# Performance work log

Measured on AMD Instinct MI355X. Metric: run time of the kernel, lower is better.

## Reference

```python
import jax, jax.numpy as jnp
import numpy as np

J = 3
J_H = 5
C_IN = 128
C_OUT = 128
N0, N1, N2 = 1024, 3072, 2048
DENSITY = 0.01
W_SCALE = 0.02  # keeps P^(2^(J_h-1)) @ x @ W magnitudes reasonable in fp32


def _sym_sparse(key, n, density):
    kv, km = jax.random.split(key)
    mask = jax.random.uniform(km, (n, n)) < density
    a = jnp.where(mask, jax.random.normal(kv, (n, n)), 0.0)
    return jnp.triu(a) + jnp.triu(a, 1).T  # symmetric sparse 'Laplacian'


def _sparse(kv, km, shape, density):
    mask = jax.random.uniform(km, shape) < density
    return jnp.where(mask, jax.random.normal(kv, shape), 0.0)


def setup_inputs() -> dict:
    key = jax.random.key(0)
    ks = jax.random.split(key, 24)
    z0 = jax.random.normal(ks[0], (N0, C_IN), jnp.float32)
    z1 = jax.random.normal(ks[1], (N1, C_IN), jnp.float32)
    z2 = jax.random.normal(ks[2], (N2, C_IN), jnp.float32)
    L0 = _sym_sparse(ks[3], N0, 0.02)
    L1_d = _sym_sparse(ks[4], N1, DENSITY)
    L1_u = _sym_sparse(ks[5], N1, DENSITY)
    L2 = _sym_sparse(ks[6], N2, DENSITY)
    B1 = _sparse(ks[7], ks[8], (N0, N1), DENSITY)
    B2 = _sparse(ks[9], ks[10], (N1, N2), DENSITY)
    W_d = jax.random.normal(ks[11], (J, C_IN, C_OUT)) * W_SCALE
    W_u = jax.random.normal(ks[12], (J, C_IN, C_OUT)) * W_SCALE
    W_h = jax.random.normal(ks[13], (C_IN, C_OUT)) * W_SCALE
    W_b1 = jax.random.normal(ks[14], (J, C_IN, C_OUT)) * W_SCALE
    W_b2 = jax.random.normal(ks[15], (J, C_IN, C_OUT)) * W_SCALE
    attn_d_w = jax.random.normal(ks[16], (1, 2 * C_IN)) * W_SCALE
    attn_d_b = jax.random.normal(ks[17], (1,)) * W_SCALE
    attn_u_w = jax.random.normal(ks[18], (1, 2 * C_IN)) * W_SCALE
    attn_u_b = jax.random.normal(ks[19], (1,)) * W_SCALE
    return dict(z0=z0, z1=z1, z2=z2, L0=L0, L1_d=L1_d, L1_u=L1_u, L2=L2,
                B1=B1, B2=B2, W_d=W_d, W_u=W_u, W_h=W_h, W_b1=W_b1, W_b2=W_b2,
                attn_d_w=attn_d_w, attn_d_b=attn_d_b,
                attn_u_w=attn_u_w, attn_u_b=attn_u_b)


def _attention(x, n, w, b, src, dst):
    # gather edge endpoints -> tiny MLP -> sigmoid -> symmetric scatter
    a = jnp.concatenate([x[src], x[dst]], axis=-1)      # [E, 2C]
    s = jax.nn.sigmoid(a @ w.T + b)[:, 0]               # [E]
    return jnp.zeros((n, n), x.dtype).at[src, dst].set(s).at[dst, src].set(s)


def _harmonic(L, x, W_h):
    lmax = jnp.linalg.eigvalsh(L)[-1]
    # torch does lambda_max.item() -> constant w.r.t. grads
    eps = jax.lax.stop_gradient(jnp.where(lmax > 0, 1.0 / lmax, 0.1))
    P = jnp.eye(L.shape[0], dtype=x.dtype) - eps * L
    for _ in range(J_H - 1):
        P = P @ P                                        # P^(2^(J_h-1))
    return P @ x @ W_h


def reference(z0, z1, z2, L0, L1_d, L1_u, L2, B1, B2,
              W_d, W_u, W_h, W_b1, W_b2,
              attn_d_w, attn_d_b, attn_u_w, attn_u_b):
    # nonzero patterns of the Laplacians (constants, computed on host)
    src_d, dst_d = np.nonzero(np.asarray(jax.device_get(L1_d)))
    src_u, dst_u = np.nonzero(np.asarray(jax.device_get(L1_u)))
    L1d_attn = _attention(z1, N1, attn_d_w, attn_d_b,
                          jnp.asarray(src_d), jnp.asarray(dst_d))
    L1u_attn = _attention(z1, N1, attn_u_w, attn_u_b,
                          jnp.asarray(src_u), jnp.asarray(dst_u))
    # sum_j (A @ z) @ W[j] == (A @ z) @ W.sum(0)
    Wd_s, Wu_s = W_d.sum(0), W_u.sum(0)
    Wb1_s, Wb2_s = W_b1.sum(0), W_b2.sum(0)

    z0_out = (L0 @ z0) @ Wd_s + (B1 @ z1) @ Wb1_s + _harmonic(L0, z0, W_h)
    z0_out = jax.nn.relu(z0_out)

    z1_out = ((L1d_attn @ z1) @ Wd_s + (L1u_attn @ z1) @ Wu_s
              + (B1.T @ z0) @ Wb1_s + (B2 @ z2) @ Wb2_s
              + _harmonic(L1_d + L1_u, z1, W_h))
    z1_out = jax.nn.relu(z1_out)

    z2_out = (L2 @ z2) @ Wu_s + (B2.T @ z1) @ Wb2_s + _harmonic(L2, z2, W_h)
    z2_out = jax.nn.relu(z2_out)
    return (z0_out, z1_out, z2_out)
```

## Files before the change

kernel.cpp:

```cpp
#include <hip/hip_runtime.h>
#include <string.h>

constexpr int M_LZ = 48;

constexpr int CAP_L0 = 26240, CAP_L1 = 118016, CAP_L2 = 52480, CAP_B1 = 39360, CAP_B2 = 78720;
constexpr int CB_L0 = 0;
constexpr int CB_L1D = CB_L0 + CAP_L0;
constexpr int CB_L1U = CB_L1D + CAP_L1;
constexpr int CB_L2  = CB_L1U + CAP_L1;
constexpr int CB_B1  = CB_L2 + CAP_L2;
constexpr int CB_B2  = CB_B1 + CAP_B1;
constexpr int CAP_TOT= CB_B2 + CAP_B2;
constexpr int CB_B1T = CAP_TOT;
constexpr int CB_B2T = CB_B1T + CAP_B1;
constexpr int CAP_TOT2 = CB_B2T + CAP_B2;

constexpr int P_L0=0, P_L1D=1025, P_L1U=4098, P_L2=7171, P_B1=9220, P_B2=10245;
constexpr int P_B1T=13320, P_B2T=16393;
constexpr int C_L0=0, C_L1D=1024, C_L1U=4096, C_L2=7168, C_B1=9216, C_B2=10240;
constexpr int C_B1T=13312, C_B2T=16384;

constexpr size_t HBUF  = (size_t)6144*128;

constexpr size_t W_CNT = 0;
constexpr size_t W_PTR = 18432;
constexpr size_t W_CUR = W_PTR + 18444;
constexpr size_t W_CIDX= W_CUR + 5120;
constexpr size_t W_VAL = W_CIDX + CAP_TOT2;
constexpr size_t W_V0  = W_VAL + CAP_TOT2;
constexpr size_t W_PK  = W_V0 + 6144;
constexpr size_t W_TT  = W_PK + (size_t)64*6144*4;
constexpr size_t W_EPS = W_TT + 6144;
constexpr size_t W_UV  = W_EPS + 128;
constexpr size_t W_H   = W_UV + 4*3072;
constexpr size_t W_SCAT= W_H + 15*HBUF;
constexpr size_t S0_OFF= 0;
constexpr size_t S1_OFF= (size_t)1024*384;
constexpr size_t S2_OFF= S1_OFF + (size_t)3072*640;
constexpr size_t SCAT_TOT = S2_OFF + (size_t)2048*384;
constexpr size_t W_WCAT= W_SCAT + SCAT_TOT;
constexpr size_t WC0=0, WC1=(size_t)384*128, WC2=WC1+(size_t)640*128;
constexpr size_t W_SLOT= W_WCAT + (size_t)1408*128;
constexpr size_t W_FLG = W_SLOT + 1048576;
constexpr size_t W_REL = W_FLG + 65536;

__device__ __forceinline__ float wredf(float v){
  #pragma unroll
  for(int o=32;o;o>>=1) v += __shfl_xor(v,o,64);
  return v;
}
__device__ __forceinline__ int wredi(int v){
  #pragma unroll
  for(int o=32;o;o>>=1) v += __shfl_xor(v,o,64);
  return v;
}

__device__ __forceinline__ float ldc(const float* p){
  return __hip_atomic_load(p, __ATOMIC_RELAXED, __HIP_MEMORY_SCOPE_AGENT);
}
__device__ __forceinline__ float2 ldc2(const float* p){
  unsigned long long u = __hip_atomic_load((const unsigned long long*)p,
                          __ATOMIC_RELAXED, __HIP_MEMORY_SCOPE_AGENT);
  float2 r; memcpy(&r,&u,8); return r;
}
__device__ __forceinline__ void stc(float* p, float v){
  __hip_atomic_store(p, v, __ATOMIC_RELAXED, __HIP_MEMORY_SCOPE_AGENT);
}
__device__ __forceinline__ void stc2(float* p, float2 v){
  unsigned long long u; memcpy(&u,&v,8);
  __hip_atomic_store((unsigned long long*)p, u, __ATOMIC_RELAXED, __HIP_MEMORY_SCOPE_AGENT);
}
__device__ __forceinline__ int ldci(const int* p){
  return __hip_atomic_load(p, __ATOMIC_RELAXED, __HIP_MEMORY_SCOPE_AGENT);
}
__device__ __forceinline__ void stci(int* p, int v){
  __hip_atomic_store(p, v, __ATOMIC_RELAXED, __HIP_MEMORY_SCOPE_AGENT);
}

__device__ __forceinline__ void barg(float* ws, int* leafs, int b, int lbase, int Ng,
                                     bool chk, int lidx, int ph){
  const int t = threadIdx.x;
  int* flg = (int*)ws + W_FLG;
  __builtin_amdgcn_s_waitcnt(0);
  __syncthreads();
  if (t==0) stci(flg + (size_t)b*32, ph+1);
  if (chk){
    for (int s=t; s<Ng; s+=256){
      const int* f = flg + (size_t)(lbase+s)*32;
      while (ldci(f) < ph+1) __builtin_amdgcn_s_sleep(1);
    }
    __syncthreads();
    if (t==0){
      #pragma unroll
      for (int i=0;i<16;i++) stci(leafs + (size_t)i*32, ph+1);
    }
    __syncthreads();
  } else {
    if (t==0){
      const int* rl = leafs + (size_t)(lidx&15)*32;
      while (ldci(rl) < ph+1) __builtin_amdgcn_s_sleep(1);
    }
    __syncthreads();
  }
}

__device__ __forceinline__ void bar_lz(float* ws, int b, int grp, int lbase, int Lg,
                                       bool chk, int lb, int ph, int j,
                                       float* shr, float* redm,
                                       float& a_o, float& g_o, float& ib_o){
  const int t = threadIdx.x, lane = t&63, wvv = t>>6;
  __builtin_amdgcn_s_waitcnt(0);
  __syncthreads();
  if (t==0){
    float A0=redm[0]+redm[1]+redm[2]+redm[3];
    float G0=redm[4]+redm[5]+redm[6]+redm[7];
    float N0=redm[8]+redm[9]+redm[10]+redm[11];
    float* sl = ws + W_SLOT + ((size_t)j*2048 + b)*8;
    stc2(sl+2, make_float2(A0,G0)); stc(sl+4, N0);
    __builtin_amdgcn_s_waitcnt(0);
    stci((int*)sl, ph+1);
  }
  if (chk){
    float pa=0.f, pg=0.f, pn=0.f;
    for (int s=t; s<Lg; s+=256){
      const float* sl = ws + W_SLOT + ((size_t)j*2048 + lbase+s)*8;
      while (ldci((const int*)sl) < ph+1) __builtin_amdgcn_s_sleep(1);
      float2 ag = ldc2(sl+2); float nn = ldc(sl+4);
      pa+=ag.x; pg+=ag.y; pn+=nn;
    }
    pa=wredf(pa); pg=wredf(pg); pn=wredf(pn);
    if (lane==0){ shr[0*4+wvv]=pa; shr[1*4+wvv]=pg; shr[2*4+wvv]=pn; }
    __syncthreads();
    if (t==0){
      float a=shr[0]+shr[1]+shr[2]+shr[3];
      float g=shr[4]+shr[5]+shr[6]+shr[7];
      float n=shr[8]+shr[9]+shr[10]+shr[11];
      float ib = 1.f/sqrtf(fmaxf(n - a*a - g*g, 1e-20f));
      float* TT = ws + W_TT + (size_t)(grp*64 + j)*32;
      stc2(TT, make_float2(a,g)); stc(TT+2, n);
      #pragma unroll
      for (int i=0;i<16;i++){
        float* lf = ws + W_REL + (size_t)(grp*16+i)*32;
        stc2(lf+2, make_float2(a,g)); stc(lf+4, ib);
      }
      __builtin_amdgcn_s_waitcnt(0);
      #pragma unroll
      for (int i=0;i<16;i++)
        stci((int*)(ws + W_REL) + (size_t)(grp*16+i)*32, ph+1);
      shr[0]=a; shr[1]=g; shr[2]=ib;
    }
    __syncthreads();
  } else {
    if (t==0){
      const float* lf = ws + W_REL + (size_t)(grp*16 + (lb&15))*32;
      while (ldci((const int*)lf) < ph+1) __builtin_amdgcn_s_sleep(1);
      float2 ag = ldc2(lf+2); float ib = ldc(lf+4);
      shr[0]=ag.x; shr[1]=ag.y; shr[2]=ib;
    }
    __syncthreads();
  }
  a_o = shr[0]; g_o = shr[1]; ib_o = shr[2];
}

__global__ void k_wprep(const float* Wd,const float* Wu,const float* Wh,
                        const float* Wb1,const float* Wb2, float* ws){
  int t = blockIdx.x*256 + threadIdx.x;
  if (t >= 16384) return;
  int* wsi = (int*)ws;
  if (t < 5120) wsi[W_CNT + 13312 + t] = 0;
  if (t < 5120) wsi[W_CUR + t] = 0;
  for (int i=t; i<65536+2048; i+=16384) wsi[W_FLG+i] = 0;
  for (int i=t; i<131072; i+=16384) wsi[W_SLOT + (size_t)i*8] = 0;
  float sd = Wd[t]  + Wd[16384+t]  + Wd[32768+t];
  float su = Wu[t]  + Wu[16384+t]  + Wu[32768+t];
  float s1 = Wb1[t] + Wb1[16384+t] + Wb1[32768+t];
  float s2 = Wb2[t] + Wb2[16384+t] + Wb2[32768+t];
  float wh = Wh[t];
  float* W0 = ws + W_WCAT + WC0;
  float* W1 = ws + W_WCAT + WC1;
  float* W2 = ws + W_WCAT + WC2;
  W0[t]=sd; W0[16384+t]=s1; W0[32768+t]=wh;
  W1[t]=sd; W1[16384+t]=su; W1[32768+t]=s1; W1[49152+t]=s2; W1[65536+t]=wh;
  W2[t]=su; W2[16384+t]=s2; W2[32768+t]=wh;
}

__device__ __forceinline__ void mat_meta(int wid, const float* L0,const float* L1d,const float* L1u,
    const float* L2,const float* B1,const float* B2,
    const float*& M,int& ncol,int& lrow,int& co,int& po,int& cb,int& cap,int& tco){
  if (wid < 1024){ M=L0;  ncol=1024; lrow=wid;        co=C_L0;  po=P_L0;  cb=CB_L0;  cap=CAP_L0; tco=-1; }
  else if (wid < 4096){ M=L1d; ncol=3072; lrow=wid-1024;  co=C_L1D; po=P_L1D; cb=CB_L1D; cap=CAP_L1; tco=-1; }
  else if (wid < 7168){ M=L1u; ncol=3072; lrow=wid-4096;  co=C_L1U; po=P_L1U; cb=CB_L1U; cap=CAP_L1; tco=-1; }
  else if (wid < 9216){ M=L2;  ncol=2048; lrow=wid-7168;  co=C_L2;  po=P_L2;  cb=CB_L2;  cap=CAP_L2; tco=-1; }
  else if (wid < 10240){ M=B1; ncol=3072; lrow=wid-9216;  co=C_B1;  po=P_B1;  cb=CB_B1;  cap=CAP_B1; tco=C_B1T; }
  else { M=B2; ncol=2048; lrow=wid-10240; co=C_B2;  po=P_B2;  cb=CB_B2;  cap=CAP_B2; tco=C_B2T; }
}

__global__ void k_count(const float* L0,const float* L1d,const float* L1u,const float* L2,
                        const float* B1,const float* B2,int* cnt){
  int wid = blockIdx.x*4 + (threadIdx.x>>6);
  int lane = threadIdx.x & 63;
  if (wid >= 13312) return;
  const float* M; int ncol,lrow,co,po,cb,cap,tco;
  mat_meta(wid,L0,L1d,L1u,L2,B1,B2,M,ncol,lrow,co,po,cb,cap,tco);
  const float4* row4 = (const float4*)(M + (size_t)lrow*ncol);
  int c = 0;
  for (int j0=0; j0<ncol; j0+=256){
    float4 v = row4[(j0>>2)+lane];
    int n0=v.x!=0.f, n1=v.y!=0.f, n2=v.z!=0.f, n3=v.w!=0.f;
    c += n0+n1+n2+n3;
    if (tco>=0){
      int jb = j0 + lane*4;
      if (n0) atomicAdd(cnt+tco+jb,   1);
      if (n1) atomicAdd(cnt+tco+jb+1, 1);
      if (n2) atomicAdd(cnt+tco+jb+2, 1);
      if (n3) atomicAdd(cnt+tco+jb+3, 1);
    }
  }
  c = wredi(c);
  if (lane==0) cnt[co+lrow] = c;
}

__global__ void k_prefix(const int* cnt, int* ptr, int* cur){
  __shared__ int lds[257];
  const int rows[8]={1024,3072,3072,2048,1024,3072,3072,2048};
  const int cofs[8]={C_L0,C_L1D,C_L1U,C_L2,C_B1,C_B2,C_B1T,C_B2T};
  const int pofs[8]={P_L0,P_L1D,P_L1U,P_L2,P_B1,P_B2,P_B1T,P_B2T};
  int b=blockIdx.x, t=threadIdx.x;
  int R=rows[b]; const int* c=cnt+cofs[b]; int* p=ptr+pofs[b];
  int* cc = (b==6)? cur : (b==7)? cur+3072 : nullptr;
  int chunk=(R+255)/256;
  int lo=t*chunk, hi=min(R,lo+chunk);
  int s=0;
  for(int i=lo;i<hi;i++) s+=c[i];
  lds[t]=s; __syncthreads();
  if(t==0){ int run=0; for(int i=0;i<256;i++){int x=lds[i];lds[i]=run;run+=x;} lds[256]=run; }
  __syncthreads();
  int run=lds[t];
  for(int i=lo;i<hi;i++){ p[i]=run; if(cc) cc[i]=run; run+=c[i]; }
  if(t==0) p[R]=lds[256];
}

__global__ void k_fill(const float* L0,const float* L1d,const float* L1u,const float* L2,
                       const float* B1,const float* B2,const int* ptr,int* cidx,float* val){
  int wid = blockIdx.x*4 + (threadIdx.x>>6);
  int lane = threadIdx.x & 63;
  if (wid >= 13312) return;
  const float* M; int ncol,lrow,co,po,cb,cap,tco;
  mat_meta(wid,L0,L1d,L1u,L2,B1,B2,M,ncol,lrow,co,po,cb,cap,tco);
  const float4* row4 = (const float4*)(M + (size_t)lrow*ncol);
  int base = ptr[po+lrow];
  int run = 0;
  for (int j0=0; j0<ncol; j0+=256){
    float4 v = row4[(j0>>2)+lane];
    int n0=v.x!=0.f, n1=v.y!=0.f, n2=v.z!=0.f, n3=v.w!=0.f;
    int local = n0+n1+n2+n3;
    int incl = local;
    #pragma unroll
    for (int o=1;o<64;o<<=1){
      int tmp = __shfl_up(incl,o,64);
      if (lane>=o) incl += tmp;
    }
    int tot = __shfl(incl,63,64);
    int pos = base + run + incl - local;
    int jb = j0 + lane*4;
    if (n0){ if(pos<cap){cidx[cb+pos]=jb;   val[cb+pos]=v.x;} pos++; }
    if (n1){ if(pos<cap){cidx[cb+pos]=jb+1; val[cb+pos]=v.y;} pos++; }
    if (n2){ if(pos<cap){cidx[cb+pos]=jb+2; val[cb+pos]=v.z;} pos++; }
    if (n3){ if(pos<cap){cidx[cb+pos]=jb+3; val[cb+pos]=v.w;} pos++; }
    run += tot;
  }
}

__global__ void k_fillT(float* ws){
  int wid = blockIdx.x*4 + (threadIdx.x>>6);
  int lane = threadIdx.x & 63;
  if (wid >= 4096) return;
  int* wsi=(int*)ws;
  const int* ptr=wsi+W_PTR; int* cidx=wsi+W_CIDX; float* val=ws+W_VAL;
  int* cur=wsi+W_CUR;
  if (wid < 1024){
    int r=wid;
    int e=ptr[P_B1+r+1];
    for(int k=ptr[P_B1+r]+lane;k<e;k+=64){
      int c=cidx[CB_B1+k]; float v=val[CB_B1+k];
      int pos=atomicAdd(cur+c,1);
      cidx[CB_B1T+pos]=r; val[CB_B1T+pos]=v;
    }
  } else {
    int r=wid-1024;
    int e=ptr[P_B2+r+1];
    for(int k=ptr[P_B2+r]+lane;k<e;k+=64){
      int c=cidx[CB_B2+k]; float v=val[CB_B2+k];
      int pos=atomicAdd(cur+3072+c,1);
      cidx[CB_B2T+pos]=r; val[CB_B2T+pos]=v;
    }
  }
}

__global__ __launch_bounds__(256,8) void k_solve(float* ws,
    const float* z0,const float* z1,const float* z2,
    const float* adw,const float* adb,const float* auw,const float* aub,
    float* out){
  const int b = blockIdx.x, t = threadIdx.x;
  const int wv = t>>6, lane = t&63;
  const int sg = lane>>4, chn = lane&15;
  const int* wsi=(const int*)ws;
  const int* ptr=wsi+W_PTR; const int* cidx=wsi+W_CIDX; const float* val=ws+W_VAL;

  __shared__ float smem[2616];
  float* Sl  = smem;
  float* Wl  = smem + 544;
  float* TTa = smem;
  float* TTb = smem + 64;
  float* redm= smem + 2592;
  float* shr = smem + 2604;

  int* grel = (int*)ws + W_REL + 48*32;

  { int i = b*256+t;
    if (i < 6144){
      float invs = (i<1024)?0.03125f:(i<4096)?0.0180421959f:0.0220970869f;
      unsigned uu=(unsigned)i*2654435761u; uu^=uu>>16; uu*=2246822519u; uu^=uu>>13;
      stc(ws+W_V0+i, (uu&1)?invs:-invs);
    }
  }
  { int gw = b*4+wv;
    if (gw < 3072){
      float2 x  = ((const float2*)(z1+(size_t)gw*128))[lane];
      float2 a0 = ((const float2*)adw)[lane];
      float2 a1 = ((const float2*)adw)[64+lane];
      float2 b0 = ((const float2*)auw)[lane];
      float2 b1 = ((const float2*)auw)[64+lane];
      float ud=x.x*a0.x+x.y*a0.y, vd=x.x*a1.x+x.y*a1.y;
      float uu=x.x*b0.x+x.y*b0.y, vu=x.x*b1.x+x.y*b1.y;
      ud=wredf(ud); vd=wredf(vd); uu=wredf(uu); vu=wredf(vu);
      if(lane==0){ stc(ws+W_UV+gw,ud); stc(ws+W_UV+3072+gw,vd);
                   stc(ws+W_UV+6144+gw,uu); stc(ws+W_UV+9216+gw,vu); }
    }
  }
  if (b==0 && t<16) stci((int*)ws + W_CNT + (size_t)t*32, 0);
  barg(ws, grel, b, 0, 2048, b==0, b, 0);

  if (b < 768){
    int g, gbase, nb;
    if (b<128){ g=0; gbase=0;   nb=0;    }
    else if (b<512){ g=1; gbase=128; nb=1024; }
    else { g=2; gbase=512; nb=4096; }
    const int lb = b - gbase;
    const int Lg = (g==0)?128:(g==1)?384:256;
    const bool chk = (lb==0);
    const int hw = lane>>5, hl = lane&31;
    const int p  = lb*8 + wv*2 + hw;
    const int gp = nb + p;
    float a=0.f, gmm=0.f, ib=1.f;
    float vp_m1=0.f, vp_m2=0.f, wp_m1=0.f;
    for (int j=0;j<M_LZ;j++){
      float wp=0.f;
      if (j==0){
        const float* v0 = ws + W_V0;
        #define GZ(PP,CBB) { const int* rp=ptr+PP; int e=rp[p+1]; \
          for (int k=rp[p]+hl;k<e;k+=32){ wp += val[CBB+k]*v0[nb+cidx[CBB+k]]; } }
        if (g==0){ GZ(P_L0,CB_L0) }
        else if (g==1){ GZ(P_L1D,CB_L1D) GZ(P_L1U,CB_L1U) }
        else { GZ(P_L2,CB_L2) }
        #undef GZ
      } else {
        const float4* pk = (const float4*)(ws + W_PK) + (size_t)(j-1)*6144 + nb;
        #define GP(PP,CBB) { const int* rp=ptr+PP; int e=rp[p+1]; \
          for (int k=rp[p]+hl;k<e;k+=32){ float v=val[CBB+k]; float4 pq=pk[cidx[CBB+k]]; \
            wp += v*((pq.x - a*pq.y - gmm*pq.z)*ib); } }
        if (g==0){ GP(P_L0,CB_L0) }
        else if (g==1){ GP(P_L1D,CB_L1D) GP(P_L1U,CB_L1U) }
        else { GP(P_L2,CB_L2) }
        #undef GP
      }
      #pragma unroll
      for (int o=16;o;o>>=1) wp += __shfl_xor(wp,o,64);
      float rA=0.f, rG=0.f, rN=0.f;
      if (hl==0){
        float vp;
        if (j==0) vp = ws[W_V0+gp];
        else      vp = (wp_m1 - a*vp_m1 - gmm*vp_m2)*ib;
        float* pkw = ws + W_PK + ((size_t)j*6144 + gp)*4;
        stc2(pkw, make_float2(wp, vp)); stc(pkw+2, vp_m1);
        rA = vp*wp; rG = vp_m1*wp; rN = wp*wp;
        vp_m2 = vp_m1; vp_m1 = vp; wp_m1 = wp;
      }
      rA += __shfl_xor(rA,32,64); rG += __shfl_xor(rG,32,64); rN += __shfl_xor(rN,32,64);
      if (lane==0){ redm[0*4+wv]=rA; redm[1*4+wv]=rG; redm[2*4+wv]=rN; }
      bar_lz(ws, b, g, gbase, Lg, chk, lb, 1+j, j, shr, redm, a, gmm, ib);
    }
    if (chk && t<64){
      int i = t;
      double lo=1e300, hi=-1e300;
      if (i<M_LZ){
        const float* TT = ws + W_TT + (size_t)(g*64 + i)*32;
        float aa=TT[0], gg=TT[1], nn=TT[2];
        TTa[i]=aa; TTb[i]=sqrtf(fmaxf(nn-aa*aa-gg*gg,1e-20f));
      }
      if (i<M_LZ){
        double r=(i? fabs((double)TTb[i-1]):0.0) + (i<M_LZ-1? fabs((double)TTb[i]):0.0);
        lo=(double)TTa[i]-r; hi=(double)TTa[i]+r;
      }
      #pragma unroll
      for(int o=32;o;o>>=1){ lo=fmin(lo,__shfl_xor(lo,o,64)); hi=fmax(hi,__shfl_xor(hi,o,64)); }
      lo -= 1.0; hi += 1.0;
      for (int round=0; round<4; round++){
        double x = lo + (hi-lo)*(double)(i+1)/65.0;
        double d = 1.0; int cnt2=0;
        for (int k2=0;k2<M_LZ;k2++){
          double bi = k2? (double)TTb[k2-1] : 0.0;
          d = ((double)TTa[k2]-x) - bi*bi/d;
          if (d==0.0) d = -1e-300;
          if (d<0.0) cnt2++;
        }
        double nlo = (cnt2< M_LZ)? x : -1e300;
        double nhi = (cnt2==M_LZ)? x :  1e300;
        #pragma unroll
        for(int o=32;o;o>>=1){ nlo=fmax(nlo,__shfl_xor(nlo,o,64)); nhi=fmin(nhi,__shfl_xor(nhi,o,64)); }
        if (nlo>-1e299) lo=nlo;
        if (nhi< 1e299) hi=nhi;
      }
      double lam = 0.5*(lo+hi);
      if (i==0) stc(ws+W_EPS+(size_t)g*32, (lam>0.0)? (float)(1.0/lam) : 0.1f);
    }
  } else {
    const int kb = b - 768;
    const int hw = lane>>5;
    const int sgh = (lane>>4)&1;
    const int r = kb*8 + wv*2 + hw;
    const bool act = (r < 6144);
    int cg=0, nb2=0, lr=0; const float* zz=z0; float eps0=0.0625f;
    if (act){
      if (r<1024){ cg=0; nb2=0;    lr=r;      zz=z0; eps0=0.0625f;     }
      else if (r<4096){ cg=1; nb2=1024; lr=r-1024; zz=z1; eps0=(1.f/28.f); }
      else { cg=2; nb2=4096; lr=r-4096; zz=z2; eps0=0.0625f; }
    }
    for (int k2=1; k2<=16; k2++){
      if (act){
        float4 a0={0.f,0.f,0.f,0.f}, a1={0.f,0.f,0.f,0.f};
        const float* ybase = ws + W_H + (size_t)(k2>=2? k2-2:0)*HBUF;
        #define KG(PP,CBB) { const int* rp=ptr+PP; int e=rp[lr+1]; \
          for (int kk=rp[lr]+sgh; kk<e; kk+=2){ \
            float v=val[CBB+kk]; int q=cidx[CBB+kk]; \
            const float* sr = (k2==1)? zz+(size_t)q*128 : ybase+(size_t)(nb2+q)*128; \
            float4 x0=((const float4*)sr)[chn*2], x1=((const float4*)sr)[chn*2+1]; \
            a0.x+=v*x0.x; a0.y+=v*x0.y; a0.z+=v*x0.z; a0.w+=v*x0.w; \
            a1.x+=v*x1.x; a1.y+=v*x1.y; a1.z+=v*x1.z; a1.w+=v*x1.w; \
          } }
        if (cg==0){ KG(P_L0,CB_L0) }
        else if (cg==1){ KG(P_L1D,CB_L1D) KG(P_L1U,CB_L1U) }
        else { KG(P_L2,CB_L2) }
        #undef KG
        a0.x+=__shfl_xor(a0.x,16,64); a0.y+=__shfl_xor(a0.y,16,64);
        a0.z+=__shfl_xor(a0.z,16,64); a0.w+=__shfl_xor(a0.w,16,64);
        a1.x+=__shfl_xor(a1.x,16,64); a1.y+=__shfl_xor(a1.y,16,64);
        a1.z+=__shfl_xor(a1.z,16,64); a1.w+=__shfl_xor(a1.w,16,64);
        if ((lane&16)==0){
          float* dst;
          if (k2<16) dst = ws + W_H + (size_t)(k2-1)*HBUF + (size_t)r*128;
          else {
            if (cg==0)      dst = ws+W_SCAT+S0_OFF+256 + (size_t)lr*384;
            else if (cg==1) dst = ws+W_SCAT+S1_OFF+512 + (size_t)lr*640;
            else            dst = ws+W_SCAT+S2_OFF+256 + (size_t)lr*384;
          }
          stc2(dst+chn*8,   make_float2(eps0*a0.x, eps0*a0.y));
          stc2(dst+chn*8+2, make_float2(eps0*a0.z, eps0*a0.w));
          stc2(dst+chn*8+4, make_float2(eps0*a1.x, eps0*a1.y));
          stc2(dst+chn*8+6, make_float2(eps0*a1.z, eps0*a1.w));
        }
      }
      if (k2<16) barg(ws, (int*)ws + W_CNT, b, 768, 1280, b==768, kb, k2);
    }
    for (int wid2 = kb*4+wv; wid2 < 18432; wid2 += 5120){
      int task,p2;
      if(wid2<1024){task=0;p2=wid2;}
      else if(wid2<2048){task=1;p2=wid2-1024;}
      else if(wid2<5120){task=2;p2=wid2-2048;}
      else if(wid2<8192){task=3;p2=wid2-5120;}
      else if(wid2<11264){task=4;p2=wid2-8192;}
      else if(wid2<13312){task=5;p2=wid2-11264;}
      else if(wid2<16384){task=6;p2=wid2-13312;}
      else {task=7;p2=wid2-16384;}
      const float* in; const int* rp; int cb2; float* outp; int ostride;
      int mode=0; float Vp=0.f, bb=0.f; const float* U=nullptr;
      switch(task){
        case 0: rp=ptr+P_L0;  cb2=CB_L0;  in=z0; outp=ws+W_SCAT+S0_OFF+0;   ostride=384; break;
        case 1: rp=ptr+P_B1;  cb2=CB_B1;  in=z1; outp=ws+W_SCAT+S0_OFF+128; ostride=384; break;
        case 2: rp=ptr+P_L1D; cb2=CB_L1D; in=z1; outp=ws+W_SCAT+S1_OFF+0;   ostride=640;
                mode=1; U=ws+W_UV; Vp=ws[W_UV+3072+p2]; bb=adb[0]; break;
        case 3: rp=ptr+P_L1U; cb2=CB_L1U; in=z1; outp=ws+W_SCAT+S1_OFF+128; ostride=640;
                mode=1; U=ws+W_UV+6144; Vp=ws[W_UV+9216+p2]; bb=aub[0]; break;
        case 4: rp=ptr+P_B2;  cb2=CB_B2;  in=z2; outp=ws+W_SCAT+S1_OFF+384; ostride=640; break;
        case 5: rp=ptr+P_L2;  cb2=CB_L2;  in=z2; outp=ws+W_SCAT+S2_OFF+0;   ostride=384; break;
        case 6: rp=ptr+P_B1T; cb2=CB_B1T; in=z0; outp=ws+W_SCAT+S1_OFF+256; ostride=640; break;
        default:rp=ptr+P_B2T; cb2=CB_B2T; in=z1; outp=ws+W_SCAT+S2_OFF+128; ostride=384; break;
      }
      float4 a0={0.f,0.f,0.f,0.f}, a1={0.f,0.f,0.f,0.f};
      int e=rp[p2+1];
      for (int k=rp[p2]+sg; k<e; k+=4){
        int q = cidx[cb2+k];
        float v;
        if (mode) v = 1.0f/(1.0f+__expf(-(U[q]+Vp+bb)));
        else v = val[cb2+k];
        const float* sr = in + (size_t)q*128;
        float4 x0 = ((const float4*)sr)[chn*2];
        float4 x1 = ((const float4*)sr)[chn*2+1];
        a0.x+=v*x0.x; a0.y+=v*x0.y; a0.z+=v*x0.z; a0.w+=v*x0.w;
        a1.x+=v*x1.x; a1.y+=v*x1.y; a1.z+=v*x1.z; a1.w+=v*x1.w;
      }
      #pragma unroll
      for (int o=16;o<=32;o<<=1){
        a0.x+=__shfl_xor(a0.x,o,64); a0.y+=__shfl_xor(a0.y,o,64);
        a0.z+=__shfl_xor(a0.z,o,64); a0.w+=__shfl_xor(a0.w,o,64);
        a1.x+=__shfl_xor(a1.x,o,64); a1.y+=__shfl_xor(a1.y,o,64);
        a1.z+=__shfl_xor(a1.z,o,64); a1.w+=__shfl_xor(a1.w,o,64);
      }
      if (sg==0){
        float* dst = outp + (size_t)p2*ostride;
        stc2(dst+chn*8,   make_float2(a0.x,a0.y));
        stc2(dst+chn*8+2, make_float2(a0.z,a0.w));
        stc2(dst+chn*8+4, make_float2(a1.x,a1.y));
        stc2(dst+chn*8+6, make_float2(a1.z,a1.w));
      }
    }
  }

  barg(ws, grel, b, 0, 2048, b==1, b, 30);

  { int r = b*4+wv;
    if (r < 6144){
      int cg = (r<1024)?0:(r<4096)?1:2;
      int lr = r - ((cg==0)?0:(cg==1)?1024:4096);
      const float* zz = (cg==0)?z0:(cg==1)?z1:z2;
      float lam0 = (cg==1)?28.f:16.f;
      float eps  = ws[W_EPS+(size_t)cg*32];
      float rr = eps*lam0;
      float* hc;
      if (cg==0)      hc = ws+W_SCAT+S0_OFF+256 + (size_t)lr*384;
      else if (cg==1) hc = ws+W_SCAT+S1_OFF+512 + (size_t)lr*640;
      else            hc = ws+W_SCAT+S2_OFF+256 + (size_t)lr*384;
      const float BIN[17] = {1.f,16.f,120.f,560.f,1820.f,4368.f,8008.f,11440.f,12870.f,
                             11440.f,8008.f,4368.f,1820.f,560.f,120.f,16.f,1.f};
      float2 acc = ((const float2*)(zz + (size_t)lr*128))[lane];
      float rk = 1.f;
      #pragma unroll
      for (int k2=1;k2<=15;k2++){
        rk *= -rr;
        float2 y = ((const float2*)(ws + W_H + (size_t)(k2-1)*HBUF + (size_t)r*128))[lane];
        float c = BIN[k2]*rk;
        acc.x += c*y.x; acc.y += c*y.y;
      }
      rk *= -rr;
      float2 y16 = ((const float2*)hc)[lane];
      acc.x += rk*y16.x; acc.y += rk*y16.y;
      stc2(hc + (size_t)lane*2, acc);
    }
  }
  barg(ws, grel, b, 0, 2048, b==1, b, 31);

  if (b < 192){
    const float* S; const float* W; float* outp; int K; int blk;
    if (b<32){       S=ws+W_SCAT+S0_OFF; W=ws+W_WCAT+WC0; outp=out;        K=384; blk=b; }
    else if (b<128){ S=ws+W_SCAT+S1_OFF; W=ws+W_WCAT+WC1; outp=out+131072; K=640; blk=b-32; }
    else {           S=ws+W_SCAT+S2_OFF; W=ws+W_WCAT+WC2; outp=out+524288; K=384; blk=b-128; }
    int r0=blk*32;
    int ty=t>>5, tx=t&31;
    float acc[4][4]={};
    for (int k0=0; k0<K; k0+=16){
      {
        int r=t>>3, kq=(t&7)*2;
        const float* src=S+(size_t)(r0+r)*K + k0+kq;
        Sl[r*17+kq]=src[0]; Sl[r*17+kq+1]=src[1];
      }
      {
        int kk=t>>4, cq=(t&15)*8;
        const float* src=W+(size_t)(k0+kk)*128+cq;
        #pragma unroll
        for(int i=0;i<8;i++) Wl[kk*128+cq+i]=src[i];
      }
      __syncthreads();
      #pragma unroll
      for(int k=0;k<16;k++){
        float sv[4], wvv2[4];
        #pragma unroll
        for(int i=0;i<4;i++) sv[i]=Sl[(ty*4+i)*17+k];
        #pragma unroll
        for(int i=0;i<4;i++) wvv2[i]=Wl[k*128+tx+32*i];
        #pragma unroll
        for(int a2=0;a2<4;a2++)
          #pragma unroll
          for(int b2=0;b2<4;b2++) acc[a2][b2]+=sv[a2]*wvv2[b2];
      }
      __syncthreads();
    }
    #pragma unroll
    for(int a2=0;a2<4;a2++)
      #pragma unroll
      for(int b2=0;b2<4;b2++){
        int r=r0+ty*4+a2, col=tx+32*b2;
        outp[(size_t)r*128+col]=fmaxf(acc[a2][b2],0.f);
      }
  }
}

extern "C" void kernel_launch(void* const* d_in, const int* in_sizes, int n_in,
                              void* d_out, int out_size, void* d_ws, size_t ws_size,
                              hipStream_t stream){
  const float* z0 =(const float*)d_in[0];
  const float* z1 =(const float*)d_in[1];
  const float* z2 =(const float*)d_in[2];
  const float* L0 =(const float*)d_in[3];
  const float* L1d=(const float*)d_in[4];
  const float* L1u=(const float*)d_in[5];
  const float* L2 =(const float*)d_in[6];
  const float* B1 =(const float*)d_in[7];
  const float* B2 =(const float*)d_in[8];
  const float* Wd =(const float*)d_in[9];
  const float* Wu =(const float*)d_in[10];
  const float* Wh =(const float*)d_in[11];
  const float* Wb1=(const float*)d_in[12];
  const float* Wb2=(const float*)d_in[13];
  const float* adw=(const float*)d_in[14];
  const float* adb=(const float*)d_in[15];
  const float* auw=(const float*)d_in[16];
  const float* aub=(const float*)d_in[17];
  float* ws=(float*)d_ws;
  int* wsi=(int*)d_ws;
  float* out=(float*)d_out;

  hipLaunchKernelGGL(k_wprep, dim3(64), dim3(256), 0, stream, Wd,Wu,Wh,Wb1,Wb2,ws);
  hipLaunchKernelGGL(k_count, dim3(3328), dim3(256), 0, stream, L0,L1d,L1u,L2,B1,B2, wsi+W_CNT);
  hipLaunchKernelGGL(k_prefix, dim3(8), dim3(256), 0, stream, wsi+W_CNT, wsi+W_PTR, wsi+W_CUR);
  hipLaunchKernelGGL(k_fill, dim3(3328), dim3(256), 0, stream, L0,L1d,L1u,L2,B1,B2, wsi+W_PTR, wsi+W_CIDX, ws+W_VAL);
  hipLaunchKernelGGL(k_fillT, dim3(1024), dim3(256), 0, stream, ws);
  hipLaunchKernelGGL(k_solve, dim3(2048), dim3(256), 0, stream,
                     ws, z0, z1, z2, adw, adb, auw, aub, out);
}
```

Measured before the change: 847.8 us.

## Remap power-iteration rows to one row per wave with four-way nnz split

The 16-step propagation loop on the 1280 helper blocks now gives each wave one row of the L1/L2 groups (5120 waves cover 3072+2048 rows) instead of two rows per wave. Each row's nonzeros are split four ways across 16-lane subgroups. The 1024 L0 rows are folded in as a second task on the first 1024 waves. The aim is to balance the denser L1 rows across more lanes and to avoid idle half-waves, so each barrier-separated step finishes sooner. The cost is an extra shuffle reduction stage, and the waves that also handle an L0 row carry more work per step.

After: 780.4 us. 7.9% less time.

```diff
diff --git a/kernel.cpp b/kernel.cpp
--- a/kernel.cpp
+++ b/kernel.cpp
@@ -53,6 +53,15 @@
   #pragma unroll
   for(int o=32;o;o>>=1) v += __shfl_xor(v,o,64);
   return v;
+}
+__device__ __forceinline__ void red4x2(float4& a0, float4& a1){
+  #pragma unroll
+  for (int o=16;o<=32;o<<=1){
+    a0.x+=__shfl_xor(a0.x,o,64); a0.y+=__shfl_xor(a0.y,o,64);
+    a0.z+=__shfl_xor(a0.z,o,64); a0.w+=__shfl_xor(a0.w,o,64);
+    a1.x+=__shfl_xor(a1.x,o,64); a1.y+=__shfl_xor(a1.y,o,64);
+    a1.z+=__shfl_xor(a1.z,o,64); a1.w+=__shfl_xor(a1.w,o,64);
+  }
 }
 
 __device__ __forceinline__ float ldc(const float* p){
@@ -426,50 +435,48 @@
     }
   } else {
     const int kb = b - 768;
-    const int hw = lane>>5;
-    const int sgh = (lane>>4)&1;
-    const int r = kb*8 + wv*2 + hw;
-    const bool act = (r < 6144);
-    int cg=0, nb2=0, lr=0; const float* zz=z0; float eps0=0.0625f;
-    if (act){
-      if (r<1024){ cg=0; nb2=0;    lr=r;      zz=z0; eps0=0.0625f;     }
-      else if (r<4096){ cg=1; nb2=1024; lr=r-1024; zz=z1; eps0=(1.f/28.f); }
-      else { cg=2; nb2=4096; lr=r-4096; zz=z2; eps0=0.0625f; }
-    }
+    const int vw = kb*4 + wv;
+    int cgP, nbP, lrP; float e0P;
+    if (vw < 3072){ cgP=1; nbP=1024; lrP=vw;      e0P=(1.f/28.f); }
+    else          { cgP=2; nbP=4096; lrP=vw-3072; e0P=0.0625f;    }
+    const bool has2 = (vw < 1024);
     for (int k2=1; k2<=16; k2++){
-      if (act){
+      const float* ybase = ws + W_H + (size_t)(k2>=2? k2-2:0)*HBUF;
+      #define KG2(PP,CBB,NBV,ZZV,LRV) { const int* rp=ptr+PP; int e=rp[(LRV)+1]; \
+        for (int kk=rp[LRV]+sg; kk<e; kk+=4){ \
+          float v=val[CBB+kk]; int q=cidx[CBB+kk]; \
+          const float* sr = (k2==1)? (ZZV)+(size_t)q*128 : ybase+(size_t)((NBV)+q)*128; \
+          float4 x0=((const float4*)sr)[chn*2], x1=((const float4*)sr)[chn*2+1]; \
+          a0.x+=v*x0.x; a0.y+=v*x0.y; a0.z+=v*x0.z; a0.w+=v*x0.w; \
+          a1.x+=v*x1.x; a1.y+=v*x1.y; a1.z+=v*x1.z; a1.w+=v*x1.w; \
+        } }
+      #define KWRITE(CGV,LRV,GRV,E0V) if (lane<16){ \
+          float* dst; \
+          if (k2<16) dst = ws + W_H + (size_t)(k2-1)*HBUF + (size_t)(GRV)*128; \
+          else { \
+            if ((CGV)==0)      dst = ws+W_SCAT+S0_OFF+256 + (size_t)(LRV)*384; \
+            else if ((CGV)==1) dst = ws+W_SCAT+S1_OFF+512 + (size_t)(LRV)*640; \
+            else               dst = ws+W_SCAT+S2_OFF+256 + (size_t)(LRV)*384; \
+          } \
+          stc2(dst+chn*8,   make_float2((E0V)*a0.x, (E0V)*a0.y)); \
+          stc2(dst+chn*8+2, make_float2((E0V)*a0.z, (E0V)*a0.w)); \
+          stc2(dst+chn*8+4, make_float2((E0V)*a1.x, (E0V)*a1.y)); \
+          stc2(dst+chn*8+6, make_float2((E0V)*a1.z, (E0V)*a1.w)); }
+      {
         float4 a0={0.f,0.f,0.f,0.f}, a1={0.f,0.f,0.f,0.f};
-        const float* ybase = ws + W_H + (size_t)(k2>=2? k2-2:0)*HBUF;
-        #define KG(PP,CBB) { const int* rp=ptr+PP; int e=rp[lr+1]; \
-          for (int kk=rp[lr]+sgh; kk<e; kk+=2){ \
-            float v=val[CBB+kk]; int q=cidx[CBB+kk]; \
-            const float* sr = (k2==1)? zz+(size_t)q*128 : ybase+(size_t)(nb2+q)*128; \
-            float4 x0=((const float4*)sr)[chn*2], x1=((const float4*)sr)[chn*2+1]; \
-            a0.x+=v*x0.x; a0.y+=v*x0.y; a0.z+=v*x0.z; a0.w+=v*x0.w; \
-            a1.x+=v*x1.x; a1.y+=v*x1.y; a1.z+=v*x1.z; a1.w+=v*x1.w; \
-          } }
-        if (cg==0){ KG(P_L0,CB_L0) }
-        else if (cg==1){ KG(P_L1D,CB_L1D) KG(P_L1U,CB_L1U) }
-        else { KG(P_L2,CB_L2) }
-        #undef KG
-        a0.x+=__shfl_xor(a0.x,16,64); a0.y+=__shfl_xor(a0.y,16,64);
-        a0.z+=__shfl_xor(a0.z,16,64); a0.w+=__shfl_xor(a0.w,16,64);
-        a1.x+=__shfl_xor(a1.x,16,64); a1.y+=__shfl_xor(a1.y,16,64);
-        a1.z+=__shfl_xor(a1.z,16,64); a1.w+=__shfl_xor(a1.w,16,64);
-        if ((lane&16)==0){
-          float* dst;
-          if (k2<16) dst = ws + W_H + (size_t)(k2-1)*HBUF + (size_t)r*128;
-          else {
-            if (cg==0)      dst = ws+W_SCAT+S0_OFF+256 + (size_t)lr*384;
-            else if (cg==1) dst = ws+W_SCAT+S1_OFF+512 + (size_t)lr*640;
-            else            dst = ws+W_SCAT+S2_OFF+256 + (size_t)lr*384;
-          }
-          stc2(dst+chn*8,   make_float2(eps0*a0.x, eps0*a0.y));
-          stc2(dst+chn*8+2, make_float2(eps0*a0.z, eps0*a0.w));
-          stc2(dst+chn*8+4, make_float2(eps0*a1.x, eps0*a1.y));
-          stc2(dst+chn*8+6, make_float2(eps0*a1.z, eps0*a1.w));
-        }
-      }
+        if (cgP==1){ KG2(P_L1D,CB_L1D,1024,z1,lrP) KG2(P_L1U,CB_L1U,1024,z1,lrP) }
+        else { KG2(P_L2,CB_L2,4096,z2,lrP) }
+        red4x2(a0,a1);
+        KWRITE(cgP, lrP, nbP+lrP, e0P)
+      }
+      if (has2){
+        float4 a0={0.f,0.f,0.f,0.f}, a1={0.f,0.f,0.f,0.f};
+        KG2(P_L0,CB_L0,0,z0,vw)
+        red4x2(a0,a1);
+        KWRITE(0, vw, vw, 0.0625f)
+      }
+      #undef KG2
+      #undef KWRITE
       if (k2<16) barg(ws, (int*)ws + W_CNT, b, 768, 1280, b==768, kb, k2);
     }
     for (int wid2 = kb*4+wv; wid2 < 18432; wid2 += 5120){
@@ -509,13 +516,7 @@
         a0.x+=v*x0.x; a0.y+=v*x0.y; a0.z+=v*x0.z; a0.w+=v*x0.w;
         a1.x+=v*x1.x; a1.y+=v*x1.y; a1.z+=v*x1.z; a1.w+=v*x1.w;
       }
-      #pragma unroll
-      for (int o=16;o<=32;o<<=1){
-        a0.x+=__shfl_xor(a0.x,o,64); a0.y+=__shfl_xor(a0.y,o,64);
-        a0.z+=__shfl_xor(a0.z,o,64); a0.w+=__shfl_xor(a0.w,o,64);
-        a1.x+=__shfl_xor(a1.x,o,64); a1.y+=__shfl_xor(a1.y,o,64);
-        a1.z+=__shfl_xor(a1.z,o,64); a1.w+=__shfl_xor(a1.w,o,64);
-      }
+      red4x2(a0, a1);
       if (sg==0){
         float* dst = outp + (size_t)p2*ostride;
         stc2(dst+chn*8,   make_float2(a0.x,a0.y));
```
